# Kernel tuning notes

Hardware: AMD Instinct MI355X
Metric: run time of the kernel (lower is better)

## Reference

```python
import jax, jax.numpy as jnp
import numpy as np

IN_FEATURES = 2048
OUT_FEATURES = 256
KERNEL_DIMS = 8
BATCH = 256


def setup_inputs() -> dict:
    key = jax.random.key(0)
    k_x, k_T = jax.random.split(key)
    x = jax.random.normal(k_x, (BATCH, IN_FEATURES), dtype=jnp.float32)
    # nn.Parameter(torch.randn(in, out, kd)) with normal_(0, 1) init
    T = jax.random.normal(k_T, (IN_FEATURES, OUT_FEATURES, KERNEL_DIMS), dtype=jnp.float32)
    return {"x": x, "T": T}


def reference(x, T):
    # M: [B, out_features, kernel_dims]
    M = jnp.einsum('bi,iok->bok', x, T)
    # Pairwise L1 distance over kernel dims: norm[i, j, o] = sum_k |M[j,o,k] - M[i,o,k]|
    # (matches torch M.unsqueeze(0) - M.permute(1,0,2,3); abs makes order irrelevant)
    norm = jnp.abs(M[None, :, :, :] - M[:, None, :, :]).sum(axis=3)  # [B, B, out]
    o_b = jnp.exp(-norm).sum(axis=0) - 1.0  # subtract self-similarity exp(0)=1
    return jnp.concatenate([x, o_b], axis=1)  # [B, in_features + out_features]
```

## Files before the change

kernel.cpp:

```cpp
#include <hip/hip_runtime.h>
#include <math.h>

#define BATCH   256
#define IN_F    2048
#define OUT_F   256
#define NCOL    2048
#define OSTRIDE 2304
#define LOG2E   1.4426950408889634f

typedef float    f32x4  __attribute__((ext_vector_type(4)));
typedef _Float16 h16x2  __attribute__((ext_vector_type(2)));
typedef __fp16   fp16x2 __attribute__((ext_vector_type(2)));
typedef unsigned short u16;
typedef unsigned int   u32;
typedef unsigned char  u8;
typedef long long      i64;

#define WT_BASE   (16u << 20)
#define XB_BASE   (24u << 20)

__device__ __forceinline__ float exp2_fast(float x) {
#if __has_builtin(__builtin_amdgcn_exp2f)
    return __builtin_amdgcn_exp2f(x);
#else
    float r; asm("v_exp_f32 %0, %1" : "=v"(r) : "v"(x)); return r;
#endif
}

__device__ __forceinline__ float hsum_neg(h16x2 s) {
#if __has_builtin(__builtin_amdgcn_fdot2)
    const h16x2 n1 = {(_Float16)-1.0f, (_Float16)-1.0f};
    return __builtin_amdgcn_fdot2(s, n1, 0.0f, false);
#else
    return -((float)s[0] + (float)s[1]);
#endif
}

__device__ __forceinline__ float bperm(int srcLane, float v) {
    return __builtin_bit_cast(float,
        __builtin_amdgcn_ds_bpermute(srcLane * 4, __builtin_bit_cast(int, v)));
}

__device__ __forceinline__ u32 pk4_fp8(float a, float b, float c, float d) {
    u32 r;
    asm("v_cvt_pk_fp8_f32 %0, %1, %2" : "=v"(r) : "v"(a), "v"(b));
    asm("v_cvt_pk_fp8_f32 %0, %1, %2 op_sel:[0,0,1]" : "+v"(r) : "v"(c), "v"(d));
    return r;
}

__global__ __launch_bounds__(256)
void k_prep(const float* __restrict__ X, const float* __restrict__ T,
            u8* __restrict__ Wt, u8* __restrict__ Xb) {
    const int b = blockIdx.x, t = threadIdx.x;
    if (b < 128) {
        const int c8 = b & 7;
        const int kg = b >> 3;
        const int p  = t & 127;
        const int C  = c8 + 8 * (p >> 4);
        const int n  = C * 32 + (p & 15) * 2;
        const int kh = (t >> 7) * 64;
        const int nt = n >> 4, n16 = n & 15;
#pragma unroll
        for (int kc = 0; kc < 8; ++kc) {
            const int kb = kg * 128 + kh + kc * 8;
            float a0[8], a1[8];
#pragma unroll
            for (int r = 0; r < 8; ++r) {
                float2 v = *(const float2*)(T + (size_t)(kb + r) * NCOL + n);
                a0[r] = v.x;
                a1[r] = v.y;
            }
            uint2 p0 = {pk4_fp8(a0[0], a0[1], a0[2], a0[3]),
                        pk4_fp8(a0[4], a0[5], a0[6], a0[7])};
            uint2 p1 = {pk4_fp8(a1[0], a1[1], a1[2], a1[3]),
                        pk4_fp8(a1[4], a1[5], a1[6], a1[7])};
            u8* dst = Wt + ((size_t)(nt * 256 + (kb >> 3)) * 16 + n16) * 8;
            *(uint2*)dst       = p0;
            *(uint2*)(dst + 8) = p1;
        }
    } else {
        const int g   = b - 128;
        const int rt  = g >> 3;
        const int kcb = (g & 7) * 32;
        const int r16 = t >> 4;
        const int kc  = kcb + (t & 15) * 2;
        const int row = rt * 16 + r16;
        const float* src = X + (size_t)row * IN_F + kc * 8;
        float v[16];
#pragma unroll
        for (int i = 0; i < 4; ++i)
            *(f32x4*)(v + i * 4) = *(const f32x4*)(src + i * 4);
        uint2 q0 = {pk4_fp8(v[0] * LOG2E, v[1] * LOG2E, v[2] * LOG2E, v[3] * LOG2E),
                    pk4_fp8(v[4] * LOG2E, v[5] * LOG2E, v[6] * LOG2E, v[7] * LOG2E)};
        uint2 q1 = {pk4_fp8(v[8] * LOG2E, v[9] * LOG2E, v[10] * LOG2E, v[11] * LOG2E),
                    pk4_fp8(v[12] * LOG2E, v[13] * LOG2E, v[14] * LOG2E, v[15] * LOG2E)};
        *(uint2*)(Xb + ((size_t)(rt * 256 + kc)     * 16 + r16) * 8) = q0;
        *(uint2*)(Xb + ((size_t)(rt * 256 + kc + 1) * 16 + r16) * 8) = q1;
    }
}

__global__ __launch_bounds__(512, 4)
void k_gemm(const u8* __restrict__ Xb, const u8* __restrict__ Wt,
            u16* __restrict__ Mh) {
    __shared__ float L[8][32][33];
    const int t = threadIdx.x, l = t & 63, kcw = t >> 6;
    const int bid = blockIdx.x;
    const int R = bid >> 6;
    const int C = bid & 63;

    const int lo = (l >> 4) * 128 + (l & 15) * 8;
    const u8* ap0 = Xb + (size_t)(R * 2) * 32768 + kcw * 4096 + lo;
    const u8* ap1 = ap0 + 32768;
    const u8* bp0 = Wt + (size_t)(C * 2) * 32768 + kcw * 4096 + lo;
    const u8* bp1 = bp0 + 32768;

    f32x4 c00 = {0.f,0.f,0.f,0.f}, c01 = {0.f,0.f,0.f,0.f};
    f32x4 c10 = {0.f,0.f,0.f,0.f}, c11 = {0.f,0.f,0.f,0.f};

#pragma unroll 8
    for (int s = 0; s < 8; ++s) {
        i64 a0 = *(const i64*)(ap0 + s * 512);
        i64 a1 = *(const i64*)(ap1 + s * 512);
        i64 b0 = *(const i64*)(bp0 + s * 512);
        i64 b1 = *(const i64*)(bp1 + s * 512);
        c00 = __builtin_amdgcn_mfma_f32_16x16x32_fp8_fp8(a0, b0, c00, 0, 0, 0);
        c01 = __builtin_amdgcn_mfma_f32_16x16x32_fp8_fp8(a0, b1, c01, 0, 0, 0);
        c10 = __builtin_amdgcn_mfma_f32_16x16x32_fp8_fp8(a1, b0, c10, 0, 0, 0);
        c11 = __builtin_amdgcn_mfma_f32_16x16x32_fp8_fp8(a1, b1, c11, 0, 0, 0);
    }

    const int lq = l >> 4, lm = l & 15;
#define PUT(acc, qi, qj) do { \
        _Pragma("unroll") \
        for (int r = 0; r < 4; ++r) \
            L[kcw][(qj) * 16 + lm][(qi) * 16 + lq * 4 + r] = acc[r]; \
    } while (0)
    PUT(c00, 0, 0); PUT(c01, 0, 1); PUT(c10, 1, 0); PUT(c11, 1, 1);
#undef PUT
    __syncthreads();

    if (t < 256) {
        const int o2 = t >> 6;
        const int jl = (t & 63) >> 1;
        const int k0 = (t & 1) * 4;
        float v[4];
#pragma unroll
        for (int i = 0; i < 4; ++i) {
            const int c = o2 * 8 + k0 + i;
            float s0 = (L[0][c][jl] + L[1][c][jl]) + (L[2][c][jl] + L[3][c][jl]);
            float s1 = (L[4][c][jl] + L[5][c][jl]) + (L[6][c][jl] + L[7][c][jl]);
            v[i] = s0 + s1;
        }
        fp16x2 p0 = __builtin_amdgcn_cvt_pkrtz(v[0], v[1]);
        fp16x2 p1 = __builtin_amdgcn_cvt_pkrtz(v[2], v[3]);
        uint2 pk = {__builtin_bit_cast(u32, p0), __builtin_bit_cast(u32, p1)};
        *(uint2*)(Mh + ((size_t)(C * 4 + o2) * 256 + R * 32 + jl) * 8 + k0) = pk;
    }
}

__global__ __launch_bounds__(1024)
void k_pair(const u16* __restrict__ Mh, const float* __restrict__ X,
            float* __restrict__ out) {
    __shared__ __align__(16) uint4 Msh[BATCH];
    __shared__ float Ps[16][256];
    const int t = threadIdx.x;
    const int g = blockIdx.x & 7, idx = blockIdx.x >> 3;
    const int o = (g + 8 * (idx >> 2)) * 4 + (idx & 3);

    if (t < 256) Msh[t] = ((const uint4*)(Mh + (size_t)o * 2048))[t];

    {
        const int row = blockIdx.x;
        *(float2*)(out + (size_t)row * OSTRIDE + t * 2) =
            *(const float2*)(X + (size_t)row * IN_F + t * 2);
    }
    __syncthreads();

    const int jg = t & 63, q = t >> 6;
    h16x2 m[4][4];
#pragma unroll
    for (int c = 0; c < 4; ++c) {
        uint4 mm = Msh[jg + 64 * c];
        m[c][0] = __builtin_bit_cast(h16x2, mm.x);
        m[c][1] = __builtin_bit_cast(h16x2, mm.y);
        m[c][2] = __builtin_bit_cast(h16x2, mm.z);
        m[c][3] = __builtin_bit_cast(h16x2, mm.w);
    }

    float acc[4] = {0.f, 0.f, 0.f, 0.f};
    const int dbase = q * 8 + 1;
#pragma unroll
    for (int ii = 0; ii < 8; ++ii) {
        const int d  = dbase + ii;
        const int dd = d & 63;
        const int dl = d >> 6;
        float e[4];
#pragma unroll
        for (int c = 0; c < 4; ++c) {
            uint4 uu = Msh[(jg + 64 * c + d) & 255];
            h16x2 d0 = __builtin_bit_cast(h16x2, uu.x) - m[c][0];
            h16x2 d1 = __builtin_bit_cast(h16x2, uu.y) - m[c][1];
            h16x2 d2 = __builtin_bit_cast(h16x2, uu.z) - m[c][2];
            h16x2 d3 = __builtin_bit_cast(h16x2, uu.w) - m[c][3];
            h16x2 e0 = __builtin_bit_cast(h16x2, __builtin_bit_cast(u32, d0) & 0x7fff7fffu);
            h16x2 e1 = __builtin_bit_cast(h16x2, __builtin_bit_cast(u32, d1) & 0x7fff7fffu);
            h16x2 e2 = __builtin_bit_cast(h16x2, __builtin_bit_cast(u32, d2) & 0x7fff7fffu);
            h16x2 e3 = __builtin_bit_cast(h16x2, __builtin_bit_cast(u32, d3) & 0x7fff7fffu);
            h16x2 s = (e0 + e1) + (e2 + e3);
            float ev = exp2_fast(hsum_neg(s));
            e[c] = ev;
            acc[c] += ev;
        }
        if (d != 128) {
            const int src = (jg - dd) & 63;
            float r0 = bperm(src, e[0]);
            float r1 = bperm(src, e[1]);
            float r2 = bperm(src, e[2]);
            float r3 = bperm(src, e[3]);
            const int rot = dl + (jg < dd ? 1 : 0);
            acc[0] += rot == 0 ? r0 : (rot == 1 ? r3 : r2);
            acc[1] += rot == 0 ? r1 : (rot == 1 ? r0 : r3);
            acc[2] += rot == 0 ? r2 : (rot == 1 ? r1 : r0);
            acc[3] += rot == 0 ? r3 : (rot == 1 ? r2 : r1);
        }
    }
#pragma unroll
    for (int c = 0; c < 4; ++c) Ps[q][jg + 64 * c] = acc[c];
    __syncthreads();

    if (t < 256) {
        float s = 0.f;
#pragma unroll
        for (int q2 = 0; q2 < 16; ++q2) s += Ps[q2][t];
        out[(size_t)t * OSTRIDE + IN_F + o] = s;
    }
}

extern "C" void kernel_launch(void* const* d_in, const int* in_sizes, int n_in,
                              void* d_out, int out_size, void* d_ws, size_t ws_size,
                              hipStream_t stream) {
    const float* x = (const float*)d_in[0];
    const float* T = (const float*)d_in[1];
    float* out = (float*)d_out;
    char* ws = (char*)d_ws;
    u16* Mh = (u16*)ws;
    u8*  Wt = (u8*)(ws + WT_BASE);
    u8*  Xb = (u8*)(ws + XB_BASE);

    k_prep<<<256, 256, 0, stream>>>(x, T, Wt, Xb);
    k_gemm<<<512, 512, 0, stream>>>(Xb, Wt, Mh);
    k_pair<<<256, 1024, 0, stream>>>(Mh, x, out);
}
```

Baseline: 23.52 us.

## Compute full pairwise matrix directly instead of exploiting symmetry with lane permutes

```diff
diff --git a/kernel.cpp b/kernel.cpp
--- a/kernel.cpp
+++ b/kernel.cpp
@@ -34,11 +34,6 @@
 #else
     return -((float)s[0] + (float)s[1]);
 #endif
-}
-
-__device__ __forceinline__ float bperm(int srcLane, float v) {
-    return __builtin_bit_cast(float,
-        __builtin_amdgcn_ds_bpermute(srcLane * 4, __builtin_bit_cast(int, v)));
 }
 
 __device__ __forceinline__ u32 pk4_fp8(float a, float b, float c, float d) {
@@ -162,7 +157,7 @@
 void k_pair(const u16* __restrict__ Mh, const float* __restrict__ X,
             float* __restrict__ out) {
     __shared__ __align__(16) uint4 Msh[BATCH];
-    __shared__ float Ps[16][256];
+    __shared__ float Ps[32][256];
     const int t = threadIdx.x;
     const int g = blockIdx.x & 7, idx = blockIdx.x >> 3;
     const int o = (g + 8 * (idx >> 2)) * 4 + (idx & 3);
@@ -176,63 +171,49 @@
     }
     __syncthreads();
 
-    const int jg = t & 63, q = t >> 6;
-    h16x2 m[4][4];
-#pragma unroll
-    for (int c = 0; c < 4; ++c) {
-        uint4 mm = Msh[jg + 64 * c];
+    const int jg = t & 31, q = t >> 5;
+    h16x2 m[8][4];
+#pragma unroll
+    for (int c = 0; c < 8; ++c) {
+        uint4 mm = Msh[jg + 32 * c];
         m[c][0] = __builtin_bit_cast(h16x2, mm.x);
         m[c][1] = __builtin_bit_cast(h16x2, mm.y);
         m[c][2] = __builtin_bit_cast(h16x2, mm.z);
         m[c][3] = __builtin_bit_cast(h16x2, mm.w);
     }
 
-    float acc[4] = {0.f, 0.f, 0.f, 0.f};
-    const int dbase = q * 8 + 1;
+    float acc[8] = {0.f, 0.f, 0.f, 0.f, 0.f, 0.f, 0.f, 0.f};
+    const int i0 = q * 8;
 #pragma unroll
     for (int ii = 0; ii < 8; ++ii) {
-        const int d  = dbase + ii;
-        const int dd = d & 63;
-        const int dl = d >> 6;
-        float e[4];
-#pragma unroll
-        for (int c = 0; c < 4; ++c) {
-            uint4 uu = Msh[(jg + 64 * c + d) & 255];
-            h16x2 d0 = __builtin_bit_cast(h16x2, uu.x) - m[c][0];
-            h16x2 d1 = __builtin_bit_cast(h16x2, uu.y) - m[c][1];
-            h16x2 d2 = __builtin_bit_cast(h16x2, uu.z) - m[c][2];
-            h16x2 d3 = __builtin_bit_cast(h16x2, uu.w) - m[c][3];
+        uint4 uu = Msh[i0 + ii];
+        const h16x2 u0 = __builtin_bit_cast(h16x2, uu.x);
+        const h16x2 u1 = __builtin_bit_cast(h16x2, uu.y);
+        const h16x2 u2 = __builtin_bit_cast(h16x2, uu.z);
+        const h16x2 u3 = __builtin_bit_cast(h16x2, uu.w);
+#pragma unroll
+        for (int c = 0; c < 8; ++c) {
+            h16x2 d0 = u0 - m[c][0];
+            h16x2 d1 = u1 - m[c][1];
+            h16x2 d2 = u2 - m[c][2];
+            h16x2 d3 = u3 - m[c][3];
             h16x2 e0 = __builtin_bit_cast(h16x2, __builtin_bit_cast(u32, d0) & 0x7fff7fffu);
             h16x2 e1 = __builtin_bit_cast(h16x2, __builtin_bit_cast(u32, d1) & 0x7fff7fffu);
             h16x2 e2 = __builtin_bit_cast(h16x2, __builtin_bit_cast(u32, d2) & 0x7fff7fffu);
             h16x2 e3 = __builtin_bit_cast(h16x2, __builtin_bit_cast(u32, d3) & 0x7fff7fffu);
             h16x2 s = (e0 + e1) + (e2 + e3);
-            float ev = exp2_fast(hsum_neg(s));
-            e[c] = ev;
-            acc[c] += ev;
+            acc[c] += exp2_fast(hsum_neg(s));
         }
-        if (d != 128) {
-            const int src = (jg - dd) & 63;
-            float r0 = bperm(src, e[0]);
-            float r1 = bperm(src, e[1]);
-            float r2 = bperm(src, e[2]);
-            float r3 = bperm(src, e[3]);
-            const int rot = dl + (jg < dd ? 1 : 0);
-            acc[0] += rot == 0 ? r0 : (rot == 1 ? r3 : r2);
-            acc[1] += rot == 0 ? r1 : (rot == 1 ? r0 : r3);
-            acc[2] += rot == 0 ? r2 : (rot == 1 ? r1 : r0);
-            acc[3] += rot == 0 ? r3 : (rot == 1 ? r2 : r1);
-        }
-    }
-#pragma unroll
-    for (int c = 0; c < 4; ++c) Ps[q][jg + 64 * c] = acc[c];
+    }
+#pragma unroll
+    for (int c = 0; c < 8; ++c) Ps[q][jg + 32 * c] = acc[c];
     __syncthreads();
 
     if (t < 256) {
         float s = 0.f;
 #pragma unroll
-        for (int q2 = 0; q2 < 16; ++q2) s += Ps[q2][t];
-        out[(size_t)t * OSTRIDE + IN_F + o] = s;
+        for (int q2 = 0; q2 < 32; ++q2) s += Ps[q2][t];
+        out[(size_t)t * OSTRIDE + IN_F + o] = s - 1.0f;
     }
 }
 
```

Result: slower. 25.39 us (+7.9%).
